# Optimization experiments

Measured on AMD Instinct MI355X. Metric: run time of the kernel, lower is better.

Reference implementation:

```python
import jax, jax.numpy as jnp
import numpy as np

VOCAB, EMBED, HIDDEN = 32000, 256, 512
B, N = 8, 2048

def setup_inputs() -> dict:
    key = jax.random.key(0)
    ks = jax.random.split(key, 8)
    s_e = 1.0  # torch Embedding default init N(0,1)
    inp = {
        'tokens': jax.random.randint(ks[0], (B, N), 0, VOCAB),
        'emb_table': jax.random.normal(ks[1], (VOCAB, EMBED), jnp.float32) * s_e,
        'W1': jax.random.normal(ks[2], (HIDDEN, EMBED), jnp.float32) * (1.0 / np.sqrt(EMBED)),
        'b1': jnp.zeros((HIDDEN,), jnp.float32),
        'W2': jax.random.normal(ks[3], (HIDDEN, HIDDEN), jnp.float32) * (1.0 / np.sqrt(HIDDEN)),
        'b2': jnp.zeros((HIDDEN,), jnp.float32),
        'Wp': jax.random.normal(ks[4], (HIDDEN, HIDDEN), jnp.float32) * (1.0 / np.sqrt(HIDDEN)),
        'bp': jnp.zeros((HIDDEN,), jnp.float32),
    }
    return inp

def reference(tokens, emb_table, W1, b1, W2, b2, Wp, bp):
    # embedding lookup: [B,N,E]
    embeds = emb_table[tokens]
    # MLP encoder: Linear->ReLU->Linear  [B,N,H]
    h = jax.nn.relu(jnp.einsum('bne,he->bnh', embeds, W1) + b1)
    hidden = jnp.einsum('bnh,gh->bng', h, W2) + b2
    # rewa witness transform
    norm = hidden / jnp.maximum(jnp.linalg.norm(hidden, axis=-1, keepdims=True), 1e-12)
    sim = jnp.einsum('bnd,bmd->bnm', norm, norm)            # [B,N,N]
    overlap = jax.nn.softplus(sim)
    weighted = jnp.einsum('bnm,bmd->bnd', overlap, hidden)  # [B,N,H]
    witness = weighted.mean(axis=1)                          # [B,H]
    return jnp.einsum('bh,gh->bg', witness, Wp) + bp
```

## Files before the change

### kernel.cpp

```cpp
#include <hip/hip_runtime.h>
#include <hip/hip_bf16.h>


typedef __bf16 bf16;
typedef __bf16 bf16x4 __attribute__((ext_vector_type(4)));
typedef __bf16 bf16x8 __attribute__((ext_vector_type(8)));
typedef float f32x4 __attribute__((ext_vector_type(4)));

#define MFMA_BF16(a, b, c) __builtin_amdgcn_mfma_f32_16x16x32_bf16((a), (b), (c), 0, 0, 0)

__device__ __forceinline__ void async_copy16(const void* gptr, void* ldsptr) {
  __builtin_amdgcn_global_load_lds(
      (const __attribute__((address_space(1))) void*)gptr,
      (__attribute__((address_space(3))) void*)ldsptr, 16, 0, 0);
}

__device__ __forceinline__ float softplus_poly(float x) {
  const float u = x * x;
  float p = fmaf(u, 3.472222e-4f, -5.208333e-3f);
  p = fmaf(p, u, 0.125f);
  return fmaf(x, 0.5f, 0.69314718f) + p * u;
}

#define STAGE16_W8(K0)                                                            \
  { _Pragma("unroll")                                                             \
    for (int i_ = 0; i_ < 2; ++i_) {                                              \
      const int c_ = t + 512 * i_;                                                \
      const int row_ = c_ >> 3;                                                   \
      const int kk_ = ((c_ & 7) ^ (row_ & 7)) * 8;                                \
      async_copy16(pA + (size_t)row_ * LDK + (kk_ + (K0)), &As[c_ * 8]);          \
      async_copy16(pB + (size_t)row_ * LDK + (kk_ + (K0)), &Bs[c_ * 8]);          \
    } }

#define COMPUTE64_W8()                                                            \
  { _Pragma("unroll")                                                             \
    for (int ks_ = 0; ks_ < 2; ++ks_) {                                           \
      const int swz_ = ((ks_ * 4 + lq) ^ (lr & 7)) * 8;                           \
      bf16x8 af_[2], bf_[4];                                                      \
      _Pragma("unroll")                                                           \
      for (int i_ = 0; i_ < 2; ++i_)                                              \
        af_[i_] = *(const bf16x8*)&As[(wm * 32 + i_ * 16 + lr) * 64 + swz_];      \
      _Pragma("unroll")                                                           \
      for (int j_ = 0; j_ < 4; ++j_)                                              \
        bf_[j_] = *(const bf16x8*)&Bs[(wn * 64 + j_ * 16 + lr) * 64 + swz_];      \
      _Pragma("unroll")                                                           \
      for (int i_ = 0; i_ < 2; ++i_)                                              \
        _Pragma("unroll")                                                         \
        for (int j_ = 0; j_ < 4; ++j_)                                            \
          acc[i_][j_] = MFMA_BF16(af_[i_], bf_[j_], acc[i_][j_]);                 \
    } }

#define KSTEP_W8(K0) STAGE16_W8(K0) __syncthreads(); COMPUTE64_W8() __syncthreads();

__global__ __launch_bounds__(256)
void fused_prep(const int* __restrict__ tokens, const float* __restrict__ emb,
                const float* __restrict__ W1, const float* __restrict__ W2,
                bf16* __restrict__ embeds_b, bf16* __restrict__ W1b, bf16* __restrict__ W2b,
                float* __restrict__ zeros )
{
  int tid = blockIdx.x * 256 + threadIdx.x;
  if (tid < 1048576) {
    const int row = tid >> 6;
    const int c4 = (tid & 63) * 4;
    const int tok = tokens[row];
    const f32x4 v = *(const f32x4*)&emb[(size_t)tok * 256 + c4];
    bf16x4 o;
    o[0] = (bf16)v[0]; o[1] = (bf16)v[1]; o[2] = (bf16)v[2]; o[3] = (bf16)v[3];
    *(bf16x4*)&embeds_b[(size_t)row * 256 + c4] = o;
    return;
  }
  tid -= 1048576;
  if (tid < 32768) {
    const f32x4 v = *(const f32x4*)&W1[(size_t)tid * 4];
    bf16x4 o;
    o[0] = (bf16)v[0]; o[1] = (bf16)v[1]; o[2] = (bf16)v[2]; o[3] = (bf16)v[3];
    *(bf16x4*)&W1b[(size_t)tid * 4] = o;
    return;
  }
  tid -= 32768;
  if (tid < 65536) {
    const f32x4 v = *(const f32x4*)&W2[(size_t)tid * 4];
    bf16x4 o;
    o[0] = (bf16)v[0]; o[1] = (bf16)v[1]; o[2] = (bf16)v[2]; o[3] = (bf16)v[3];
    *(bf16x4*)&W2b[(size_t)tid * 4] = o;
    return;
  }
  tid -= 65536;
  if (tid < 9216)
    *(f32x4*)&zeros[(size_t)tid * 4] = (f32x4){0.f, 0.f, 0.f, 0.f};
}

template <bool RELU, bool SQ, int K>
__global__ __launch_bounds__(512)
void gemm_bt(const bf16* __restrict__ A, const bf16* __restrict__ Bw,
             const float* __restrict__ bias, bf16* __restrict__ C,
             float* __restrict__ sq, int N)
{
  __shared__ __align__(16) bf16 As[128 * 64];
  __shared__ __align__(16) bf16 Bs[128 * 64];
  const int m0 = blockIdx.x * 128;
  const int n0 = blockIdx.y * 128;
  const int t = threadIdx.x;
  const int lane = t & 63;
  const int w = t >> 6;
  const int wm = w >> 1, wn = w & 1;
  const int lr = lane & 15;
  const int lq = lane >> 4;
  const bf16* pA = A + (size_t)m0 * K;
  const bf16* pB = Bw + (size_t)n0 * K;
  const int LDK = K;

  f32x4 acc[2][4];
#pragma unroll
  for (int i = 0; i < 2; ++i)
#pragma unroll
    for (int j = 0; j < 4; ++j)
      acc[i][j] = (f32x4){0.f, 0.f, 0.f, 0.f};

  KSTEP_W8(0) KSTEP_W8(64) KSTEP_W8(128) KSTEP_W8(192)
  if constexpr (K > 256) { KSTEP_W8(256) KSTEP_W8(320) KSTEP_W8(384) KSTEP_W8(448) }

  float bv4[4];
#pragma unroll
  for (int j = 0; j < 4; ++j) {
    const int col = n0 + wn * 64 + j * 16 + lr;
    const float bv = bias[col];
    bv4[j] = bv;
#pragma unroll
    for (int i = 0; i < 2; ++i) {
      const int rbase = m0 + wm * 32 + i * 16 + lq * 4;
#pragma unroll
      for (int r = 0; r < 4; ++r) {
        float v = acc[i][j][r] + bv;
        if (RELU) v = fmaxf(v, 0.0f);
        C[(size_t)(rbase + r) * N + col] = (bf16)v;
      }
    }
  }
  if (SQ) {
#pragma unroll
    for (int i = 0; i < 2; ++i)
#pragma unroll
      for (int r = 0; r < 4; ++r) {
        float s2 = 0.f;
#pragma unroll
        for (int j = 0; j < 4; ++j) {
          const float v = acc[i][j][r] + bv4[j];
          s2 += v * v;
        }
        s2 += __shfl_xor(s2, 1, 64);
        s2 += __shfl_xor(s2, 2, 64);
        s2 += __shfl_xor(s2, 4, 64);
        s2 += __shfl_xor(s2, 8, 64);
        if (lr == 0)
          atomicAdd(&sq[m0 + wm * 32 + i * 16 + lq * 4 + r], s2);
      }
  }
}

__global__ __launch_bounds__(512)
void sim_colsum(const bf16* __restrict__ hidden, const float* __restrict__ sq,
                float* __restrict__ colsum)
{
  __shared__ __align__(16) bf16 As[128 * 64];
  __shared__ __align__(16) bf16 Bs[128 * 64];
  float* colacc = (float*)As;
  float* rowacc = (float*)As + 512;

  const int b = blockIdx.x;
  const int p = blockIdx.y;
  int I = (int)((33.0f - sqrtf((float)(1089 - 8 * p))) * 0.5f);
  while (p < I * 16 - ((I - 1) * I) / 2) --I;
  while (p >= (I + 1) * 16 - (I * (I + 1)) / 2) ++I;
  const int J = I + p - (I * 16 - ((I - 1) * I) / 2);
  const bool diag = (I == J);
  const bf16* base = hidden + (size_t)b * (2048 * 512);
  const float* sqb = sq + (size_t)b * 2048;
  float* csb = colsum + (size_t)b * 2048;
  const int n0 = I * 128;
  const int m0 = J * 128;
  const int t = threadIdx.x, lane = t & 63, w = t >> 6;
  const int wm = w >> 1, wn = w & 1, lr = lane & 15, lq = lane >> 4;
  const bf16* pA = base + (size_t)n0 * 512;
  const bf16* pB = base + (size_t)m0 * 512;
  const int LDK = 512;

  f32x4 acc[2][4];
#pragma unroll
  for (int i = 0; i < 2; ++i)
#pragma unroll
    for (int j = 0; j < 4; ++j)
      acc[i][j] = (f32x4){0.f, 0.f, 0.f, 0.f};

  KSTEP_W8(0) KSTEP_W8(64) KSTEP_W8(128) KSTEP_W8(192)
  KSTEP_W8(256) KSTEP_W8(320) KSTEP_W8(384) KSTEP_W8(448)

  f32x4 rv[2];
#pragma unroll
  for (int i = 0; i < 2; ++i) {
    const f32x4 s4 = *(const f32x4*)&sqb[n0 + wm * 32 + i * 16 + lq * 4];
#pragma unroll
    for (int u = 0; u < 4; ++u) rv[i][u] = rsqrtf(fmaxf(s4[u], 1e-24f));
  }
  float csum[4];
  float rsum[2][4];
#pragma unroll
  for (int j = 0; j < 4; ++j) csum[j] = 0.f;
#pragma unroll
  for (int i = 0; i < 2; ++i)
#pragma unroll
    for (int r = 0; r < 4; ++r) rsum[i][r] = 0.f;

#pragma unroll
  for (int j = 0; j < 4; ++j) {
    const float cv = rsqrtf(fmaxf(sqb[m0 + wn * 64 + j * 16 + lr], 1e-24f));
#pragma unroll
    for (int i = 0; i < 2; ++i)
#pragma unroll
      for (int r = 0; r < 4; ++r) {
        const float x = acc[i][j][r] * rv[i][r] * cv;
        const float s = softplus_poly(x);
        csum[j] += s;
        rsum[i][r] += s;
      }
  }
#pragma unroll
  for (int j = 0; j < 4; ++j) {
    float s = csum[j];
    s += __shfl_xor(s, 16, 64);
    s += __shfl_xor(s, 32, 64);
    if (lq == 0) colacc[wm * 128 + wn * 64 + j * 16 + lr] = s;
  }
  if (!diag) {
#pragma unroll
    for (int i = 0; i < 2; ++i)
#pragma unroll
      for (int r = 0; r < 4; ++r) {
        float s = rsum[i][r];
        s += __shfl_xor(s, 1, 64);
        s += __shfl_xor(s, 2, 64);
        s += __shfl_xor(s, 4, 64);
        s += __shfl_xor(s, 8, 64);
        if (lr == 0) rowacc[wn * 128 + wm * 32 + i * 16 + lq * 4 + r] = s;
      }
  }
  __syncthreads();
  if (t < 128) {
    atomicAdd(&csb[m0 + t], colacc[t] + colacc[128 + t] + colacc[256 + t] + colacc[384 + t]);
  } else if (t < 256 && !diag) {
    const int rr = t - 128;
    atomicAdd(&csb[n0 + rr], rowacc[rr] + rowacc[128 + rr]);
  }
}

__global__ __launch_bounds__(256)
void witness_partial(const float* __restrict__ colsum, const bf16* __restrict__ hidden,
                     float* __restrict__ witness)
{
  const int mc = blockIdx.x;
  const int b  = blockIdx.y;
  const int t = threadIdx.x;
  const int msub = t >> 6;
  const int dg = t & 63;
  const bf16* hb = hidden + (size_t)b * (2048 * 512);
  const float* cp = colsum + (size_t)b * 2048;
  float acc[8];
#pragma unroll
  for (int u = 0; u < 8; ++u) acc[u] = 0.f;
  const int mbeg = mc * 64 + msub * 16;
#pragma unroll 4
  for (int i = 0; i < 16; ++i) {
    const int m = mbeg + i;
    const float cw = cp[m];
    const bf16x8 v = *(const bf16x8*)&hb[(size_t)m * 512 + dg * 8];
#pragma unroll
    for (int u = 0; u < 8; ++u) acc[u] += cw * (float)v[u];
  }
  __shared__ float red[4][512];
#pragma unroll
  for (int u = 0; u < 8; ++u) red[msub][dg * 8 + u] = acc[u];
  __syncthreads();
  if (msub == 0) {
#pragma unroll
    for (int u = 0; u < 8; ++u) {
      const int d = dg * 8 + u;
      atomicAdd(&witness[(size_t)b * 512 + d],
                red[0][d] + red[1][d] + red[2][d] + red[3][d]);
    }
  }
}

__global__ __launch_bounds__(64)
void final_proj(const float* __restrict__ witness, const float* __restrict__ Wp,
                const float* __restrict__ bpv, float* __restrict__ out)
{
  const int b = blockIdx.x >> 3;
  const int gc = blockIdx.x & 7;
  const int g = gc * 64 + threadIdx.x;
  __shared__ float wit[512];
#pragma unroll
  for (int u = 0; u < 8; ++u)
    wit[threadIdx.x * 8 + u] = witness[(size_t)b * 512 + threadIdx.x * 8 + u];
  __syncthreads();
  const float* wrow = Wp + (size_t)g * 512;
  float acc = 0.f;
  for (int d0 = 0; d0 < 512; d0 += 4) {
    const f32x4 v = *(const f32x4*)&wrow[d0];
#pragma unroll
    for (int u = 0; u < 4; ++u) acc += v[u] * wit[d0 + u];
  }
  out[(size_t)b * 512 + g] = bpv[g] + acc * (1.0f / 2048.0f);
}

extern "C" void kernel_launch(void* const* d_in, const int* in_sizes, int n_in,
                              void* d_out, int out_size, void* d_ws, size_t ws_size,
                              hipStream_t stream) {
  (void)in_sizes; (void)n_in; (void)out_size; (void)ws_size;
  const int*   tokens = (const int*)d_in[0];
  const float* emb    = (const float*)d_in[1];
  const float* W1     = (const float*)d_in[2];
  const float* b1     = (const float*)d_in[3];
  const float* W2     = (const float*)d_in[4];
  const float* b2     = (const float*)d_in[5];
  const float* Wp     = (const float*)d_in[6];
  const float* bp     = (const float*)d_in[7];
  float* out = (float*)d_out;

  char* w = (char*)d_ws;
  bf16*  embeds_b = (bf16*)(w);
  bf16*  W1_b     = (bf16*)(w + (size_t) 8 * 1024 * 1024);
  bf16*  W2_b     = (bf16*)(w + (size_t) 9 * 1024 * 1024);
  bf16*  h_buf    = (bf16*)(w + (size_t)10 * 1024 * 1024);
  bf16*  hidden   = (bf16*)(w + (size_t)26 * 1024 * 1024);
  char*  zbase    =        (w + (size_t)42 * 1024 * 1024);
  float* sq       = (float*)(zbase);
  float* colsum   = (float*)(zbase + 64 * 1024);
  float* witness  = (float*)(zbase + 128 * 1024);

  fused_prep<<<4516, 256, 0, stream>>>(tokens, emb, W1, W2, embeds_b, W1_b, W2_b, sq);
  gemm_bt<true,  false, 256><<<dim3(128, 4), 512, 0, stream>>>(embeds_b, W1_b, b1, h_buf, nullptr, 512);
  gemm_bt<false, true,  512><<<dim3(128, 4), 512, 0, stream>>>(h_buf, W2_b, b2, hidden, sq, 512);
  sim_colsum<<<dim3(8, 136), 512, 0, stream>>>(hidden, sq, colsum);
  witness_partial<<<dim3(32, 8), 256, 0, stream>>>(colsum, hidden, witness);
  final_proj<<<64, 64, 0, stream>>>(witness, Wp, bp, out);
}
```

Before: 161.7 us.

## Fuse final projection into witness kernel and skip duplicate B load on diagonal tiles

The witness reduction and final projection now run in one kernel: a per-batch atomic counter picks the last block, which then performs the Wp projection, so the separate final_proj launch goes away. In sim_colsum, diagonal tiles load only the A tile and read B fragments from the same LDS buffer, which halves global-to-LDS traffic for those tiles. The zeroing region in fused_prep grows to cover the counters. The cost is that a single block per batch does the whole 512x512 projection serially, and the threadfence/counter pattern adds extra synchronization.

```diff
diff --git a/kernel.cpp b/kernel.cpp
--- a/kernel.cpp
+++ b/kernel.cpp
@@ -32,7 +32,18 @@
       async_copy16(pB + (size_t)row_ * LDK + (kk_ + (K0)), &Bs[c_ * 8]);          \
     } }
 
-#define COMPUTE64_W8()                                                            \
+#define STAGE16_SIM(K0)                                                           \
+  { _Pragma("unroll")                                                             \
+    for (int i_ = 0; i_ < 2; ++i_) {                                              \
+      const int c_ = t + 512 * i_;                                                \
+      const int row_ = c_ >> 3;                                                   \
+      const int kk_ = ((c_ & 7) ^ (row_ & 7)) * 8;                                \
+      async_copy16(pA + (size_t)row_ * 512 + (kk_ + (K0)), &As[c_ * 8]);          \
+      if (!diag)                                                                  \
+        async_copy16(pB + (size_t)row_ * 512 + (kk_ + (K0)), &Bs[c_ * 8]);        \
+    } }
+
+#define COMPUTE64_W8(BSRC)                                                        \
   { _Pragma("unroll")                                                             \
     for (int ks_ = 0; ks_ < 2; ++ks_) {                                           \
       const int swz_ = ((ks_ * 4 + lq) ^ (lr & 7)) * 8;                           \
@@ -42,7 +53,7 @@
         af_[i_] = *(const bf16x8*)&As[(wm * 32 + i_ * 16 + lr) * 64 + swz_];      \
       _Pragma("unroll")                                                           \
       for (int j_ = 0; j_ < 4; ++j_)                                              \
-        bf_[j_] = *(const bf16x8*)&Bs[(wn * 64 + j_ * 16 + lr) * 64 + swz_];      \
+        bf_[j_] = *(const bf16x8*)&BSRC[(wn * 64 + j_ * 16 + lr) * 64 + swz_];    \
       _Pragma("unroll")                                                           \
       for (int i_ = 0; i_ < 2; ++i_)                                              \
         _Pragma("unroll")                                                         \
@@ -50,7 +61,8 @@
           acc[i_][j_] = MFMA_BF16(af_[i_], bf_[j_], acc[i_][j_]);                 \
     } }
 
-#define KSTEP_W8(K0) STAGE16_W8(K0) __syncthreads(); COMPUTE64_W8() __syncthreads();
+#define KSTEP_W8(K0)  STAGE16_W8(K0)  __syncthreads(); COMPUTE64_W8(Bs)    __syncthreads();
+#define KSTEP_SIM(K0) STAGE16_SIM(K0) __syncthreads(); COMPUTE64_W8(ldsB) __syncthreads();
 
 __global__ __launch_bounds__(256)
 void fused_prep(const int* __restrict__ tokens, const float* __restrict__ emb,
@@ -86,7 +98,7 @@
     return;
   }
   tid -= 65536;
-  if (tid < 9216)
+  if (tid < 9218)
     *(f32x4*)&zeros[(size_t)tid * 4] = (f32x4){0.f, 0.f, 0.f, 0.f};
 }
 
@@ -183,7 +195,7 @@
   const int wm = w >> 1, wn = w & 1, lr = lane & 15, lq = lane >> 4;
   const bf16* pA = base + (size_t)n0 * 512;
   const bf16* pB = base + (size_t)m0 * 512;
-  const int LDK = 512;
+  const bf16* ldsB = diag ? As : Bs;
 
   f32x4 acc[2][4];
 #pragma unroll
@@ -192,8 +204,8 @@
     for (int j = 0; j < 4; ++j)
       acc[i][j] = (f32x4){0.f, 0.f, 0.f, 0.f};
 
-  KSTEP_W8(0) KSTEP_W8(64) KSTEP_W8(128) KSTEP_W8(192)
-  KSTEP_W8(256) KSTEP_W8(320) KSTEP_W8(384) KSTEP_W8(448)
+  KSTEP_SIM(0) KSTEP_SIM(64) KSTEP_SIM(128) KSTEP_SIM(192)
+  KSTEP_SIM(256) KSTEP_SIM(320) KSTEP_SIM(384) KSTEP_SIM(448)
 
   f32x4 rv[2];
 #pragma unroll
@@ -254,8 +266,10 @@
 }
 
 __global__ __launch_bounds__(256)
-void witness_partial(const float* __restrict__ colsum, const bf16* __restrict__ hidden,
-                     float* __restrict__ witness)
+void witness_final(const float* __restrict__ colsum, const bf16* __restrict__ hidden,
+                   float* __restrict__ witness, int* __restrict__ counters,
+                   const float* __restrict__ Wp, const float* __restrict__ bpv,
+                   float* __restrict__ out)
 {
   const int mc = blockIdx.x;
   const int b  = blockIdx.y;
@@ -268,7 +282,7 @@
 #pragma unroll
   for (int u = 0; u < 8; ++u) acc[u] = 0.f;
   const int mbeg = mc * 64 + msub * 16;
-#pragma unroll 4
+#pragma unroll
   for (int i = 0; i < 16; ++i) {
     const int m = mbeg + i;
     const float cw = cp[m];
@@ -288,28 +302,28 @@
                 red[0][d] + red[1][d] + red[2][d] + red[3][d]);
     }
   }
-}
-
-__global__ __launch_bounds__(64)
-void final_proj(const float* __restrict__ witness, const float* __restrict__ Wp,
-                const float* __restrict__ bpv, float* __restrict__ out)
-{
-  const int b = blockIdx.x >> 3;
-  const int gc = blockIdx.x & 7;
-  const int g = gc * 64 + threadIdx.x;
-  __shared__ float wit[512];
-#pragma unroll
-  for (int u = 0; u < 8; ++u)
-    wit[threadIdx.x * 8 + u] = witness[(size_t)b * 512 + threadIdx.x * 8 + u];
+  __threadfence();
+  __shared__ int is_last;
+  if (t == 0) is_last = (atomicAdd(&counters[b], 1) == 31) ? 1 : 0;
   __syncthreads();
-  const float* wrow = Wp + (size_t)g * 512;
-  float acc = 0.f;
-  for (int d0 = 0; d0 < 512; d0 += 4) {
-    const f32x4 v = *(const f32x4*)&wrow[d0];
-#pragma unroll
-    for (int u = 0; u < 4; ++u) acc += v[u] * wit[d0 + u];
-  }
-  out[(size_t)b * 512 + g] = bpv[g] + acc * (1.0f / 2048.0f);
+  if (!is_last) return;
+  __threadfence();
+  float* wit = &red[0][0];
+  wit[t] = witness[(size_t)b * 512 + t];
+  wit[t + 256] = witness[(size_t)b * 512 + t + 256];
+  __syncthreads();
+#pragma unroll
+  for (int gi = 0; gi < 2; ++gi) {
+    const int g = t + gi * 256;
+    const float* wrow = Wp + (size_t)g * 512;
+    float a = 0.f;
+    for (int d0 = 0; d0 < 512; d0 += 4) {
+      const f32x4 v = *(const f32x4*)&wrow[d0];
+#pragma unroll
+      for (int u = 0; u < 4; ++u) a += v[u] * wit[d0 + u];
+    }
+    out[(size_t)b * 512 + g] = bpv[g] + a * (1.0f / 2048.0f);
+  }
 }
 
 extern "C" void kernel_launch(void* const* d_in, const int* in_sizes, int n_in,
@@ -336,11 +350,11 @@
   float* sq       = (float*)(zbase);
   float* colsum   = (float*)(zbase + 64 * 1024);
   float* witness  = (float*)(zbase + 128 * 1024);
-
-  fused_prep<<<4516, 256, 0, stream>>>(tokens, emb, W1, W2, embeds_b, W1_b, W2_b, sq);
+  int*   counters = (int*)  (zbase + 144 * 1024);
+
+  fused_prep<<<4517, 256, 0, stream>>>(tokens, emb, W1, W2, embeds_b, W1_b, W2_b, sq);
   gemm_bt<true,  false, 256><<<dim3(128, 4), 512, 0, stream>>>(embeds_b, W1_b, b1, h_buf, nullptr, 512);
   gemm_bt<false, true,  512><<<dim3(128, 4), 512, 0, stream>>>(h_buf, W2_b, b2, hidden, sq, 512);
   sim_colsum<<<dim3(8, 136), 512, 0, stream>>>(hidden, sq, colsum);
-  witness_partial<<<dim3(32, 8), 256, 0, stream>>>(colsum, hidden, witness);
-  final_proj<<<64, 64, 0, stream>>>(witness, Wp, bp, out);
-}
+  witness_final<<<dim3(32, 8), 256, 0, stream>>>(colsum, hidden, witness, counters, Wp, bp, out);
+}
```

Measured after the change: 194.8 us. +20.5%, slower.
